# Kernel tuning notes

Hardware: AMD Instinct MI355X
Metric: run time of the kernel (lower is better)

Reference implementation:

```python
import jax, jax.numpy as jnp
import numpy as np

MAX_ORDERS = 8
HIDDEN = 128
B, P = 64, 1024
FREQ_SCALE = 500.0  # Hz range for synthetic peaks
TOL = 2.0           # harmonic match tolerance from source


def setup_inputs() -> dict:
    key = jax.random.key(0)
    ks = jax.random.split(key, 6)
    peak_frequencies = jax.random.uniform(ks[0], (B, P), dtype=jnp.float32) * FREQ_SCALE
    peak_magnitudes = jax.random.normal(ks[1], (B, P), dtype=jnp.float32)
    def lin(k, fan_in, fan_out):
        return jax.random.normal(k, (fan_in, fan_out), dtype=jnp.float32) * (1.0 / np.sqrt(fan_in))
    W1 = lin(ks[2], 2, HIDDEN);        b1 = jnp.zeros((HIDDEN,), jnp.float32)
    W2 = lin(ks[3], HIDDEN, HIDDEN);   b2 = jnp.zeros((HIDDEN,), jnp.float32)
    W3 = lin(ks[4], HIDDEN, MAX_ORDERS); b3 = jnp.zeros((MAX_ORDERS,), jnp.float32)
    return {"peak_frequencies": peak_frequencies, "peak_magnitudes": peak_magnitudes,
            "W1": W1, "b1": b1, "W2": W2, "b2": b2, "W3": W3, "b3": b3}


def _fundamental_freq(freqs, mags):
    """Vectorized form of the triple-nested harmonic-matching loop.
    Returns the fundamental frequency of the LAST batch element, faithfully
    reproducing the original code (which overwrites fundamental_freq per batch)."""
    valid = mags > 0.0                                   # (B,P)
    # matched[b,i,j] = exists order in [2, max_orders] with |f_j - f_i*order| < TOL
    matched = jnp.zeros(freqs.shape[:1] + (freqs.shape[1], freqs.shape[1]), dtype=bool)
    for order in range(2, MAX_ORDERS + 1):
        matched = matched | (jnp.abs(freqs[:, None, :] - freqs[:, :, None] * order) < TOL)
    eye = jnp.eye(freqs.shape[1], dtype=bool)[None]      # exclude j == i
    harmonics = jnp.sum(matched & valid[:, None, :] & ~eye, axis=2)  # (B,P) int counts
    cand = valid & (harmonics > 0)                       # candidate peaks
    any_cand = jnp.any(cand, axis=1)                     # (B,)
    # lexicographic max over (harmonics, magnitude); argmax breaks ties by first index,
    # matching Python's stable sort over i-ascending candidate lists.
    h_masked = jnp.where(cand, harmonics, -1)
    max_h = jnp.max(h_masked, axis=1, keepdims=True)
    best = cand & (h_masked == max_h)
    mag_masked = jnp.where(best, mags, -jnp.inf)
    idx_cand = jnp.argmax(mag_masked, axis=1)
    idx_fallback = jnp.argmax(mags, axis=1)
    idx = jnp.where(any_cand, idx_cand, idx_fallback)    # (B,)
    fund = jnp.take_along_axis(freqs, idx[:, None], axis=1)[:, 0]
    return fund[-1]


def reference(peak_frequencies, peak_magnitudes, W1, b1, W2, b2, W3, b3):
    # peak_detector MLP (eval mode: dropout is identity)
    x = jnp.stack([peak_frequencies, peak_magnitudes], axis=-1)   # (B,P,2)
    h = jax.nn.relu(x @ W1 + b1)
    h = jax.nn.relu(h @ W2 + b2)
    order_probs = h @ W3 + b3                                     # (B,P,max_orders)
    fundamental_freq = _fundamental_freq(peak_frequencies, peak_magnitudes)
    return (order_probs, fundamental_freq)
```

## Files before the change

kernel.cpp:

```cpp
#include <hip/hip_runtime.h>

#define HID   128
#define PNUM  1024
#define LASTB 63
#define BP    (64 * PNUM)
#define HBLK  128
#define NBLK  512
#define PPB   128
#define WS    136

typedef __attribute__((ext_vector_type(8))) short short8;
typedef __attribute__((ext_vector_type(4))) float f32x4;

__device__ __forceinline__ unsigned short f2bf(float x) {
    unsigned u = __float_as_uint(x);
    return (unsigned short)((u + 0x7FFFu + ((u >> 16) & 1u)) >> 16);
}

__device__ __forceinline__ unsigned long long umax64(unsigned long long a,
                                                     unsigned long long b) {
    return a > b ? a : b;
}

__global__ __launch_bounds__(256) void fused(
    const float* __restrict__ freqs, const float* __restrict__ mags,
    const float* __restrict__ W1, const float* __restrict__ b1,
    const float* __restrict__ W2, const float* __restrict__ b2,
    const float* __restrict__ W3, const float* __restrict__ b3,
    float* __restrict__ out, unsigned int* __restrict__ ticket,
    int* __restrict__ cnt)
{
    __shared__ unsigned short sW2T[HID * WS];
    __shared__ unsigned short sW3T[16 * WS];
    __shared__ unsigned short sH2[4][16 * WS];
    __shared__ float sf[PNUM], sm[PNUM];
    __shared__ unsigned long long sc[256], sfb[256];
    __shared__ int sLast;

    const int t = threadIdx.x;
    const int b = blockIdx.x;

    if (b < HBLK) {
        const float* fb = freqs + (size_t)LASTB * PNUM;
        const float* mb = mags  + (size_t)LASTB * PNUM;
#pragma unroll
        for (int r = 0; r < 4; ++r) {
            sf[t + 256 * r] = fb[t + 256 * r];
            sm[t + 256 * r] = mb[t + 256 * r];
        }
        __syncthreads();

        const int il = t >> 5;
        const int jc = t & 31;
        const int i  = b * 8 + il;
        const float fi = sf[i];
        float fo[7];
#pragma unroll
        for (int o = 0; o < 7; ++o) fo[o] = __fmul_rn(fi, (float)(o + 2));

        int c = 0;
#pragma unroll 4
        for (int jj = 0; jj < 32; ++jj) {
            const int j = jj * 32 + jc;
            const float fj = sf[j];
            bool match = false;
#pragma unroll
            for (int o = 0; o < 7; ++o)
                match = match || (fabsf(__fsub_rn(fj, fo[o])) < 2.0f);
            if (match && (sm[j] > 0.0f) && (j != i)) ++c;
        }
#pragma unroll
        for (int off = 16; off > 0; off >>= 1) c += __shfl_down(c, off, 32);
        if (jc == 0)
            __hip_atomic_store(&cnt[i], c, __ATOMIC_RELAXED,
                               __HIP_MEMORY_SCOPE_AGENT);
        __syncthreads();

        if (t == 0) {
            __threadfence();
            const unsigned int old = __hip_atomic_fetch_add(
                ticket, 1u, __ATOMIC_ACQ_REL, __HIP_MEMORY_SCOPE_AGENT);
            sLast = (old == HBLK - 1) ? 1 : 0;
        }
        __syncthreads();

        if (sLast) {
            __threadfence();
            unsigned long long ck = 0ull, fk = 0ull;
#pragma unroll
            for (int r = 0; r < 4; ++r) {
                const int i2 = t + 256 * r;
                const float mi = sm[i2];
                const int h = __hip_atomic_load(&cnt[i2], __ATOMIC_RELAXED,
                                                __HIP_MEMORY_SCOPE_AGENT);
                const unsigned mbits = __float_as_uint(mi);
                if (mi > 0.0f && h > 0) {
                    const unsigned long long k =
                        ((unsigned long long)h << 42) |
                        ((unsigned long long)mbits << 10) |
                        (unsigned long long)(1023 - i2);
                    ck = umax64(ck, k);
                }
                const unsigned mo =
                    (mbits & 0x80000000u) ? ~mbits : (mbits | 0x80000000u);
                const unsigned long long k2 =
                    ((unsigned long long)mo << 10) |
                    (unsigned long long)(1023 - i2);
                fk = umax64(fk, k2);
            }
            sc[t] = ck;
            sfb[t] = fk;
            __syncthreads();
            for (int s = 128; s > 0; s >>= 1) {
                if (t < s) {
                    sc[t]  = umax64(sc[t],  sc[t + s]);
                    sfb[t] = umax64(sfb[t], sfb[t + s]);
                }
                __syncthreads();
            }
            if (t == 0) {
                const unsigned long long k = sc[0] ? sc[0] : sfb[0];
                const int idx = 1023 - (int)(k & 1023ull);
                out[(size_t)BP * 8] = sf[idx];
            }
        }
    }

    {
        const float4* __restrict__ w2v = reinterpret_cast<const float4*>(W2);
#pragma unroll
        for (int rep = 0; rep < 16; ++rep) {
            const int e  = rep * 256 + t;
            const int k  = e >> 5;
            const int n0 = (e & 31) * 4;
            const float4 v = w2v[e];
            sW2T[(n0 + 0) * WS + k] = f2bf(v.x);
            sW2T[(n0 + 1) * WS + k] = f2bf(v.y);
            sW2T[(n0 + 2) * WS + k] = f2bf(v.z);
            sW2T[(n0 + 3) * WS + k] = f2bf(v.w);
        }
    }
    {
#pragma unroll
        for (int rep = 0; rep < 5; ++rep) {
            const int idx = rep * 256 + t;
            if (idx < 8 * WS) sW3T[8 * WS + idx] = 0;
        }
#pragma unroll
        for (int rep = 0; rep < 4; ++rep) {
            const int e = rep * 256 + t;
            const int k = e >> 3, o = e & 7;
            sW3T[o * WS + k] = f2bf(W3[e]);
        }
    }

    const int w    = t >> 6;
    const int lane = t & 63;
    const int cc   = lane & 15;
    const int q    = lane >> 4;
    const int pb   = b * PPB + w * 32;

    short8 af[2][4];
#pragma unroll
    for (int mt = 0; mt < 2; ++mt) {
        const int p = pb + mt * 16 + cc;
        const float fv = freqs[p];
        const float mv = mags[p];
#pragma unroll
        for (int kc = 0; kc < 4; ++kc) {
            const int k0 = kc * 32 + q * 8;
            const float4 wa0 = *(const float4*)&W1[k0];
            const float4 wa1 = *(const float4*)&W1[k0 + 4];
            const float4 wb0 = *(const float4*)&W1[HID + k0];
            const float4 wb1 = *(const float4*)&W1[HID + k0 + 4];
            const float4 bb0 = *(const float4*)&b1[k0];
            const float4 bb1 = *(const float4*)&b1[k0 + 4];
            float hv[8];
            hv[0] = fmaxf(fmaf(fv, wa0.x, fmaf(mv, wb0.x, bb0.x)), 0.0f);
            hv[1] = fmaxf(fmaf(fv, wa0.y, fmaf(mv, wb0.y, bb0.y)), 0.0f);
            hv[2] = fmaxf(fmaf(fv, wa0.z, fmaf(mv, wb0.z, bb0.z)), 0.0f);
            hv[3] = fmaxf(fmaf(fv, wa0.w, fmaf(mv, wb0.w, bb0.w)), 0.0f);
            hv[4] = fmaxf(fmaf(fv, wa1.x, fmaf(mv, wb1.x, bb1.x)), 0.0f);
            hv[5] = fmaxf(fmaf(fv, wa1.y, fmaf(mv, wb1.y, bb1.y)), 0.0f);
            hv[6] = fmaxf(fmaf(fv, wa1.z, fmaf(mv, wb1.z, bb1.z)), 0.0f);
            hv[7] = fmaxf(fmaf(fv, wa1.w, fmaf(mv, wb1.w, bb1.w)), 0.0f);
#pragma unroll
            for (int j = 0; j < 8; ++j) af[mt][kc][j] = (short)f2bf(hv[j]);
        }
    }

    float b2v[8];
#pragma unroll
    for (int nt = 0; nt < 8; ++nt) b2v[nt] = b2[nt * 16 + cc];
    const float b3v = (cc < 8) ? b3[cc] : 0.0f;

    __syncthreads();

    short8 bw3[4];
#pragma unroll
    for (int kc = 0; kc < 4; ++kc)
        bw3[kc] = *(const short8*)&sW3T[cc * WS + kc * 32 + q * 8];

    f32x4 acc[2][8];
#pragma unroll
    for (int mt = 0; mt < 2; ++mt)
#pragma unroll
        for (int nt = 0; nt < 8; ++nt) {
            f32x4 z = {0.0f, 0.0f, 0.0f, 0.0f};
            acc[mt][nt] = z;
        }

#pragma unroll
    for (int nt = 0; nt < 8; ++nt)
#pragma unroll
        for (int kc = 0; kc < 4; ++kc) {
            const short8 bf =
                *(const short8*)&sW2T[(nt * 16 + cc) * WS + kc * 32 + q * 8];
            acc[0][nt] = __builtin_amdgcn_mfma_f32_16x16x32_bf16(
                af[0][kc], bf, acc[0][nt], 0, 0, 0);
            acc[1][nt] = __builtin_amdgcn_mfma_f32_16x16x32_bf16(
                af[1][kc], bf, acc[1][nt], 0, 0, 0);
        }

    unsigned short* __restrict__ myH2 = sH2[w];
#pragma unroll
    for (int mt = 0; mt < 2; ++mt) {
#pragma unroll
        for (int nt = 0; nt < 8; ++nt) {
            const f32x4 v = acc[mt][nt];
#pragma unroll
            for (int r = 0; r < 4; ++r)
                myH2[(q * 4 + r) * WS + nt * 16 + cc] =
                    f2bf(fmaxf(v[r] + b2v[nt], 0.0f));
        }
        f32x4 oa = {0.0f, 0.0f, 0.0f, 0.0f};
#pragma unroll
        for (int kc = 0; kc < 4; ++kc) {
            const short8 a3 = *(const short8*)&myH2[cc * WS + kc * 32 + q * 8];
            oa = __builtin_amdgcn_mfma_f32_16x16x32_bf16(a3, bw3[kc], oa, 0, 0, 0);
        }
        if (cc < 8) {
            const int pg = pb + mt * 16 + q * 4;
#pragma unroll
            for (int r = 0; r < 4; ++r)
                out[(size_t)(pg + r) * 8 + cc] = oa[r] + b3v;
        }
    }
}

extern "C" void kernel_launch(void* const* d_in, const int* in_sizes, int n_in,
                              void* d_out, int out_size, void* d_ws, size_t ws_size,
                              hipStream_t stream) {
    const float* freqs = (const float*)d_in[0];
    const float* mags  = (const float*)d_in[1];
    const float* W1    = (const float*)d_in[2];
    const float* b1    = (const float*)d_in[3];
    const float* W2    = (const float*)d_in[4];
    const float* b2    = (const float*)d_in[5];
    const float* W3    = (const float*)d_in[6];
    const float* b3    = (const float*)d_in[7];
    float* out = (float*)d_out;

    unsigned int* ticket = (unsigned int*)d_ws;
    int* cnt = (int*)((char*)d_ws + 256);

    hipMemsetAsync(d_ws, 0, 4, stream);
    fused<<<NBLK, 256, 0, stream>>>(freqs, mags, W1, b1, W2, b2, W3, b3,
                                    out, ticket, cnt);
}
```

Baseline: 96.67 us.

## Spread harmonic counting across all blocks and defer final reduction to last block

```diff
diff --git a/kernel.cpp b/kernel.cpp
--- a/kernel.cpp
+++ b/kernel.cpp
@@ -1,10 +1,10 @@
 #include <hip/hip_runtime.h>
+#include <hip/hip_bf16.h>
 
 #define HID   128
 #define PNUM  1024
 #define LASTB 63
 #define BP    (64 * PNUM)
-#define HBLK  128
 #define NBLK  512
 #define PPB   128
 #define WS    136
@@ -15,6 +15,13 @@
 __device__ __forceinline__ unsigned short f2bf(float x) {
     unsigned u = __float_as_uint(x);
     return (unsigned short)((u + 0x7FFFu + ((u >> 16) & 1u)) >> 16);
+}
+
+__device__ __forceinline__ unsigned pk2(float a, float b) {
+    __hip_bfloat162 h = __float22bfloat162_rn(make_float2(a, b));
+    union { __hip_bfloat162 h2; unsigned u; } c;
+    c.h2 = h;
+    return c.u;
 }
 
 __device__ __forceinline__ unsigned long long umax64(unsigned long long a,
@@ -35,95 +42,17 @@
     __shared__ unsigned short sH2[4][16 * WS];
     __shared__ float sf[PNUM], sm[PNUM];
     __shared__ unsigned long long sc[256], sfb[256];
+    __shared__ int sRed[4];
     __shared__ int sLast;
 
     const int t = threadIdx.x;
     const int b = blockIdx.x;
 
-    if (b < HBLK) {
-        const float* fb = freqs + (size_t)LASTB * PNUM;
-        const float* mb = mags  + (size_t)LASTB * PNUM;
-#pragma unroll
-        for (int r = 0; r < 4; ++r) {
-            sf[t + 256 * r] = fb[t + 256 * r];
-            sm[t + 256 * r] = mb[t + 256 * r];
-        }
-        __syncthreads();
-
-        const int il = t >> 5;
-        const int jc = t & 31;
-        const int i  = b * 8 + il;
-        const float fi = sf[i];
-        float fo[7];
-#pragma unroll
-        for (int o = 0; o < 7; ++o) fo[o] = __fmul_rn(fi, (float)(o + 2));
-
-        int c = 0;
-#pragma unroll 4
-        for (int jj = 0; jj < 32; ++jj) {
-            const int j = jj * 32 + jc;
-            const float fj = sf[j];
-            bool match = false;
-#pragma unroll
-            for (int o = 0; o < 7; ++o)
-                match = match || (fabsf(__fsub_rn(fj, fo[o])) < 2.0f);
-            if (match && (sm[j] > 0.0f) && (j != i)) ++c;
-        }
-#pragma unroll
-        for (int off = 16; off > 0; off >>= 1) c += __shfl_down(c, off, 32);
-        if (jc == 0)
-            __hip_atomic_store(&cnt[i], c, __ATOMIC_RELAXED,
-                               __HIP_MEMORY_SCOPE_AGENT);
-        __syncthreads();
-
-        if (t == 0) {
-            __threadfence();
-            const unsigned int old = __hip_atomic_fetch_add(
-                ticket, 1u, __ATOMIC_ACQ_REL, __HIP_MEMORY_SCOPE_AGENT);
-            sLast = (old == HBLK - 1) ? 1 : 0;
-        }
-        __syncthreads();
-
-        if (sLast) {
-            __threadfence();
-            unsigned long long ck = 0ull, fk = 0ull;
-#pragma unroll
-            for (int r = 0; r < 4; ++r) {
-                const int i2 = t + 256 * r;
-                const float mi = sm[i2];
-                const int h = __hip_atomic_load(&cnt[i2], __ATOMIC_RELAXED,
-                                                __HIP_MEMORY_SCOPE_AGENT);
-                const unsigned mbits = __float_as_uint(mi);
-                if (mi > 0.0f && h > 0) {
-                    const unsigned long long k =
-                        ((unsigned long long)h << 42) |
-                        ((unsigned long long)mbits << 10) |
-                        (unsigned long long)(1023 - i2);
-                    ck = umax64(ck, k);
-                }
-                const unsigned mo =
-                    (mbits & 0x80000000u) ? ~mbits : (mbits | 0x80000000u);
-                const unsigned long long k2 =
-                    ((unsigned long long)mo << 10) |
-                    (unsigned long long)(1023 - i2);
-                fk = umax64(fk, k2);
-            }
-            sc[t] = ck;
-            sfb[t] = fk;
-            __syncthreads();
-            for (int s = 128; s > 0; s >>= 1) {
-                if (t < s) {
-                    sc[t]  = umax64(sc[t],  sc[t + s]);
-                    sfb[t] = umax64(sfb[t], sfb[t + s]);
-                }
-                __syncthreads();
-            }
-            if (t == 0) {
-                const unsigned long long k = sc[0] ? sc[0] : sfb[0];
-                const int idx = 1023 - (int)(k & 1023ull);
-                out[(size_t)BP * 8] = sf[idx];
-            }
-        }
+    {
+        const float4* fb4 = reinterpret_cast<const float4*>(freqs + (size_t)LASTB * PNUM);
+        const float4* mb4 = reinterpret_cast<const float4*>(mags  + (size_t)LASTB * PNUM);
+        reinterpret_cast<float4*>(sf)[t] = fb4[t];
+        reinterpret_cast<float4*>(sm)[t] = mb4[t];
     }
 
     {
@@ -153,6 +82,38 @@
             sW3T[o * WS + k] = f2bf(W3[e]);
         }
     }
+    __syncthreads();
+
+    {
+        const int i_loc = t >> 7;
+        const int jc    = t & 127;
+        const int i     = b * 2 + i_loc;
+        const float fi  = sf[i];
+        float fo[7];
+#pragma unroll
+        for (int o = 0; o < 7; ++o) fo[o] = __fmul_rn(fi, (float)(o + 2));
+
+        int c = 0;
+#pragma unroll
+        for (int jj = 0; jj < 8; ++jj) {
+            const int j = jj * 128 + jc;
+            const float fj = sf[j];
+            bool match = false;
+#pragma unroll
+            for (int o = 0; o < 7; ++o)
+                match = match || (fabsf(__fsub_rn(fj, fo[o])) < 2.0f);
+            if (match && (sm[j] > 0.0f) && (j != i)) ++c;
+        }
+#pragma unroll
+        for (int off = 32; off > 0; off >>= 1) c += __shfl_down(c, off, 64);
+        if ((t & 63) == 0) sRed[t >> 6] = c;
+    }
+    __syncthreads();
+    if ((t & 127) == 0) {
+        const int i = b * 2 + (t >> 7);
+        __hip_atomic_store(&cnt[i], sRed[(t >> 6)] + sRed[(t >> 6) + 1],
+                           __ATOMIC_RELAXED, __HIP_MEMORY_SCOPE_AGENT);
+    }
 
     const int w    = t >> 6;
     const int lane = t & 63;
@@ -160,41 +121,51 @@
     const int q    = lane >> 4;
     const int pb   = b * PPB + w * 32;
 
+    const int p0 = pb + cc;
+    const int p1 = pb + 16 + cc;
+    const float f0 = freqs[p0], m0 = mags[p0];
+    const float f1 = freqs[p1], m1 = mags[p1];
+
     short8 af[2][4];
 #pragma unroll
-    for (int mt = 0; mt < 2; ++mt) {
-        const int p = pb + mt * 16 + cc;
-        const float fv = freqs[p];
-        const float mv = mags[p];
-#pragma unroll
-        for (int kc = 0; kc < 4; ++kc) {
-            const int k0 = kc * 32 + q * 8;
-            const float4 wa0 = *(const float4*)&W1[k0];
-            const float4 wa1 = *(const float4*)&W1[k0 + 4];
-            const float4 wb0 = *(const float4*)&W1[HID + k0];
-            const float4 wb1 = *(const float4*)&W1[HID + k0 + 4];
-            const float4 bb0 = *(const float4*)&b1[k0];
-            const float4 bb1 = *(const float4*)&b1[k0 + 4];
-            float hv[8];
-            hv[0] = fmaxf(fmaf(fv, wa0.x, fmaf(mv, wb0.x, bb0.x)), 0.0f);
-            hv[1] = fmaxf(fmaf(fv, wa0.y, fmaf(mv, wb0.y, bb0.y)), 0.0f);
-            hv[2] = fmaxf(fmaf(fv, wa0.z, fmaf(mv, wb0.z, bb0.z)), 0.0f);
-            hv[3] = fmaxf(fmaf(fv, wa0.w, fmaf(mv, wb0.w, bb0.w)), 0.0f);
-            hv[4] = fmaxf(fmaf(fv, wa1.x, fmaf(mv, wb1.x, bb1.x)), 0.0f);
-            hv[5] = fmaxf(fmaf(fv, wa1.y, fmaf(mv, wb1.y, bb1.y)), 0.0f);
-            hv[6] = fmaxf(fmaf(fv, wa1.z, fmaf(mv, wb1.z, bb1.z)), 0.0f);
-            hv[7] = fmaxf(fmaf(fv, wa1.w, fmaf(mv, wb1.w, bb1.w)), 0.0f);
-#pragma unroll
-            for (int j = 0; j < 8; ++j) af[mt][kc][j] = (short)f2bf(hv[j]);
-        }
+    for (int kc = 0; kc < 4; ++kc) {
+        const int k0 = kc * 32 + q * 8;
+        const float4 wa0 = *(const float4*)&W1[k0];
+        const float4 wa1 = *(const float4*)&W1[k0 + 4];
+        const float4 wb0 = *(const float4*)&W1[HID + k0];
+        const float4 wb1 = *(const float4*)&W1[HID + k0 + 4];
+        const float4 bb0 = *(const float4*)&b1[k0];
+        const float4 bb1 = *(const float4*)&b1[k0 + 4];
+        float h0[8], h1v[8];
+        h0[0] = fmaxf(fmaf(f0, wa0.x, fmaf(m0, wb0.x, bb0.x)), 0.0f);
+        h0[1] = fmaxf(fmaf(f0, wa0.y, fmaf(m0, wb0.y, bb0.y)), 0.0f);
+        h0[2] = fmaxf(fmaf(f0, wa0.z, fmaf(m0, wb0.z, bb0.z)), 0.0f);
+        h0[3] = fmaxf(fmaf(f0, wa0.w, fmaf(m0, wb0.w, bb0.w)), 0.0f);
+        h0[4] = fmaxf(fmaf(f0, wa1.x, fmaf(m0, wb1.x, bb1.x)), 0.0f);
+        h0[5] = fmaxf(fmaf(f0, wa1.y, fmaf(m0, wb1.y, bb1.y)), 0.0f);
+        h0[6] = fmaxf(fmaf(f0, wa1.z, fmaf(m0, wb1.z, bb1.z)), 0.0f);
+        h0[7] = fmaxf(fmaf(f0, wa1.w, fmaf(m0, wb1.w, bb1.w)), 0.0f);
+        h1v[0] = fmaxf(fmaf(f1, wa0.x, fmaf(m1, wb0.x, bb0.x)), 0.0f);
+        h1v[1] = fmaxf(fmaf(f1, wa0.y, fmaf(m1, wb0.y, bb0.y)), 0.0f);
+        h1v[2] = fmaxf(fmaf(f1, wa0.z, fmaf(m1, wb0.z, bb0.z)), 0.0f);
+        h1v[3] = fmaxf(fmaf(f1, wa0.w, fmaf(m1, wb0.w, bb0.w)), 0.0f);
+        h1v[4] = fmaxf(fmaf(f1, wa1.x, fmaf(m1, wb1.x, bb1.x)), 0.0f);
+        h1v[5] = fmaxf(fmaf(f1, wa1.y, fmaf(m1, wb1.y, bb1.y)), 0.0f);
+        h1v[6] = fmaxf(fmaf(f1, wa1.z, fmaf(m1, wb1.z, bb1.z)), 0.0f);
+        h1v[7] = fmaxf(fmaf(f1, wa1.w, fmaf(m1, wb1.w, bb1.w)), 0.0f);
+        union { short8 s; unsigned u[4]; } u0, u1;
+        u0.u[0] = pk2(h0[0], h0[1]);  u0.u[1] = pk2(h0[2], h0[3]);
+        u0.u[2] = pk2(h0[4], h0[5]);  u0.u[3] = pk2(h0[6], h0[7]);
+        u1.u[0] = pk2(h1v[0], h1v[1]); u1.u[1] = pk2(h1v[2], h1v[3]);
+        u1.u[2] = pk2(h1v[4], h1v[5]); u1.u[3] = pk2(h1v[6], h1v[7]);
+        af[0][kc] = u0.s;
+        af[1][kc] = u1.s;
     }
 
     float b2v[8];
 #pragma unroll
     for (int nt = 0; nt < 8; ++nt) b2v[nt] = b2[nt * 16 + cc];
     const float b3v = (cc < 8) ? b3[cc] : 0.0f;
-
-    __syncthreads();
 
     short8 bw3[4];
 #pragma unroll
@@ -209,7 +180,6 @@
             f32x4 z = {0.0f, 0.0f, 0.0f, 0.0f};
             acc[mt][nt] = z;
         }
-
 #pragma unroll
     for (int nt = 0; nt < 8; ++nt)
 #pragma unroll
@@ -244,6 +214,56 @@
 #pragma unroll
             for (int r = 0; r < 4; ++r)
                 out[(size_t)(pg + r) * 8 + cc] = oa[r] + b3v;
+        }
+    }
+
+    __syncthreads();
+    if (t == 0) {
+        __threadfence();
+        const unsigned int old = __hip_atomic_fetch_add(
+            ticket, 1u, __ATOMIC_ACQ_REL, __HIP_MEMORY_SCOPE_AGENT);
+        sLast = (old == NBLK - 1) ? 1 : 0;
+    }
+    __syncthreads();
+
+    if (sLast) {
+        __threadfence();
+        unsigned long long ck = 0ull, fk = 0ull;
+#pragma unroll
+        for (int r = 0; r < 4; ++r) {
+            const int i2 = t + 256 * r;
+            const float mi = sm[i2];
+            const int h = __hip_atomic_load(&cnt[i2], __ATOMIC_RELAXED,
+                                            __HIP_MEMORY_SCOPE_AGENT);
+            const unsigned mbits = __float_as_uint(mi);
+            if (mi > 0.0f && h > 0) {
+                const unsigned long long k =
+                    ((unsigned long long)h << 42) |
+                    ((unsigned long long)mbits << 10) |
+                    (unsigned long long)(1023 - i2);
+                ck = umax64(ck, k);
+            }
+            const unsigned mo =
+                (mbits & 0x80000000u) ? ~mbits : (mbits | 0x80000000u);
+            const unsigned long long k2 =
+                ((unsigned long long)mo << 10) |
+                (unsigned long long)(1023 - i2);
+            fk = umax64(fk, k2);
+        }
+        sc[t] = ck;
+        sfb[t] = fk;
+        __syncthreads();
+        for (int s = 128; s > 0; s >>= 1) {
+            if (t < s) {
+                sc[t]  = umax64(sc[t],  sc[t + s]);
+                sfb[t] = umax64(sfb[t], sfb[t + s]);
+            }
+            __syncthreads();
+        }
+        if (t == 0) {
+            const unsigned long long k = sc[0] ? sc[0] : sfb[0];
+            const int idx = 1023 - (int)(k & 1023ull);
+            out[(size_t)BP * 8] = sf[idx];
         }
     }
 }
```

Measured after the change: 112.2 us. 1.16x slower.
